# Kernel tuning notes

Hardware: AMD Instinct MI355X
Metric: run time of the kernel (lower is better)

## Reference

```python
import jax, jax.numpy as jnp
import numpy as np

HEADS = 16
EMBED = 1024
D_K = EMBED // HEADS


def setup_inputs() -> dict:
    key = jax.random.key(0)
    ks = jax.random.split(key, 11)
    B, S, E = 4, 2048, EMBED
    sc = 0.02
    return {
        "query": jax.random.normal(ks[0], (B, S, E), jnp.float32),
        "key_": jax.random.normal(ks[1], (B, S, E), jnp.float32),
        "value": jax.random.normal(ks[2], (B, S, E), jnp.float32),
        "Wq": jax.random.normal(ks[3], (E, E), jnp.float32) * sc,
        "bq": jnp.zeros((E,), jnp.float32),
        "Wk": jax.random.normal(ks[4], (E, E), jnp.float32) * sc,
        "bk": jnp.zeros((E,), jnp.float32),
        "Wv": jax.random.normal(ks[5], (E, E), jnp.float32) * sc,
        "bv": jnp.zeros((E,), jnp.float32),
        "Wo": jax.random.normal(ks[6], (E, D_K), jnp.float32) * sc,  # out: Linear(heads*d_k -> d_k)
        "bo": jnp.zeros((D_K,), jnp.float32),
    }


def reference(query, key_, value, Wq, bq, Wk, bk, Wv, bv, Wo, bo):
    B, S, E = query.shape
    H, Dk = HEADS, D_K
    # QKV projections
    q = query @ Wq + bq          # (B,S,E)
    k = key_ @ Wk + bk
    v = value @ Wv + bv
    # split heads -> (B,H,S,Dk)
    q = q.reshape(B, S, H, Dk).transpose(0, 2, 1, 3)
    k = k.reshape(B, S, H, Dk).transpose(0, 2, 1, 3)
    v = v.reshape(B, S, H, Dk).transpose(0, 2, 1, 3)
    # attention: softmax(QK^T / sqrt(d_k)) V
    scores = jnp.einsum("bhqd,bhkd->bhqk", q, k) / jnp.sqrt(jnp.asarray(Dk, q.dtype))
    attn = jax.nn.softmax(scores, axis=-1)
    ctx = jnp.einsum("bhqk,bhkd->bhqd", attn, v)
    ctx = ctx.transpose(0, 2, 1, 3).reshape(B, S, E)
    # output projection (E -> d_k, as in source)
    return ctx @ Wo + bo
```

## Files before the change

kernel.cpp:

```cpp
#include <hip/hip_runtime.h>
#include <hip/hip_bf16.h>
#include <cstdint>
#include <cstddef>

#define DEVI static __device__ __forceinline__

typedef unsigned short u16;
typedef unsigned int u32;
typedef __bf16 bf16_t;
typedef __bf16 bf16x8 __attribute__((ext_vector_type(8)));
typedef float f32x4 __attribute__((ext_vector_type(4)));
typedef float f32x16 __attribute__((ext_vector_type(16)));

union U16x8 { uint4 u; bf16x8 v; };
union PU { u32 w[4]; bf16x8 v; };

#define QSCALE 0.1803368801111204f

DEVI void gload_lds16(const void* g, void* l) {
  __builtin_amdgcn_global_load_lds((const __attribute__((address_space(1))) void*)g,
                                   (__attribute__((address_space(3))) void*)l, 16, 0, 0);
}
DEVI void wait_vmcnt0() { asm volatile("s_waitcnt vmcnt(0)" ::: "memory"); }

DEVI u32 cvt_pk_bf16(float lo, float hi) {
  u32 r;
  asm("v_cvt_pk_bf16_f32 %0, %1, %2" : "=v"(r) : "v"(lo), "v"(hi));
  return r;
}

DEVI void permswap(u32& a, u32& b) {
  asm("v_permlane32_swap_b32 %0, %1" : "+v"(a), "+v"(b));
}

DEVI f32x16 mfma32(bf16x8 a, bf16x8 b, f32x16 c) {
  return __builtin_amdgcn_mfma_f32_32x32x16_bf16(a, b, c, 0, 0, 0);
}

DEVI bf16x8 lds_frag(const char* base, int row, int koff, int swz) {
  U16x8 u;
  u.u = *(const uint4*)(base + row * 128 + (koff ^ swz));
  return u.v;
}

DEVI void transpose_body(const float* __restrict__ src, bf16_t* __restrict__ dst,
                         int R, int C, float scale, int tile, int t,
                         u16 (*tileb)[65]) {
  int tiles_c = C >> 6;
  int tc = tile % tiles_c;
  int tr = tile / tiles_c;
  int r0 = tr << 6, c0 = tc << 6;
  #pragma unroll
  for (int p = 0; p < 4; ++p) {
    int idx = t + p * 256;
    int i = idx >> 4, j4 = (idx & 15) * 4;
    float4 f = *(const float4*)(src + (size_t)(r0 + i) * C + c0 + j4);
    tileb[i][j4 + 0] = __builtin_bit_cast(u16, (bf16_t)(f.x * scale));
    tileb[i][j4 + 1] = __builtin_bit_cast(u16, (bf16_t)(f.y * scale));
    tileb[i][j4 + 2] = __builtin_bit_cast(u16, (bf16_t)(f.z * scale));
    tileb[i][j4 + 3] = __builtin_bit_cast(u16, (bf16_t)(f.w * scale));
  }
  __syncthreads();
  #pragma unroll
  for (int p = 0; p < 2; ++p) {
    int idx = t + p * 256;
    int j = idx >> 3, i0 = (idx & 7) * 8;
    u16 us[8];
    #pragma unroll
    for (int e = 0; e < 8; ++e) us[e] = tileb[i0 + e][j];
    uint4 o;
    o.x = (u32)us[0] | ((u32)us[1] << 16);
    o.y = (u32)us[2] | ((u32)us[3] << 16);
    o.z = (u32)us[4] | ((u32)us[5] << 16);
    o.w = (u32)us[6] | ((u32)us[7] << 16);
    *(uint4*)((u16*)dst + (size_t)(c0 + j) * R + r0 + i0) = o;
  }
}

__global__ __launch_bounds__(256) void k_prep(
    const float* __restrict__ qa, const float* __restrict__ ka, const float* __restrict__ va,
    const float* __restrict__ Wq, const float* __restrict__ Wk,
    const float* __restrict__ Wv, const float* __restrict__ Wo,
    bf16_t* __restrict__ Abf,
    bf16_t* __restrict__ WqT, bf16_t* __restrict__ WkT,
    bf16_t* __restrict__ WvT, bf16_t* __restrict__ WoT) {
  __shared__ u16 tileb[64][65];
  const int bid = blockIdx.x;
  const int t = threadIdx.x;
  if (bid < 3072) {
    int which = bid >> 10;
    int bb = bid & 1023;
    const float* s = which == 0 ? qa : which == 1 ? ka : va;
    u16* d = (u16*)Abf + (size_t)which * 8192 * 1024;
    size_t base = ((size_t)bb * 256 + t) * 8;
    #pragma unroll
    for (int p = 0; p < 4; ++p) {
      size_t i = base + (size_t)p * 2097152;
      float4 f0 = *(const float4*)(s + i);
      float4 f1 = *(const float4*)(s + i + 4);
      uint4 o;
      o.x = cvt_pk_bf16(f0.x, f0.y); o.y = cvt_pk_bf16(f0.z, f0.w);
      o.z = cvt_pk_bf16(f1.x, f1.y); o.w = cvt_pk_bf16(f1.z, f1.w);
      *(uint4*)(d + i) = o;
    }
  } else {
    int r = bid - 3072;
    if (r < 256)      transpose_body(Wq, WqT, 1024, 1024, QSCALE, r,       t, tileb);
    else if (r < 512) transpose_body(Wk, WkT, 1024, 1024, 1.0f,   r - 256, t, tileb);
    else if (r < 768) transpose_body(Wv, WvT, 1024, 1024, 1.0f,   r - 512, t, tileb);
    else              transpose_body(Wo, WoT, 1024, 64,   1.0f,   r - 768, t, tileb);
  }
}

template<bool PRE>
__global__ __launch_bounds__(256) void k_proj_gemm(
    const float* __restrict__ Aq, const float* __restrict__ Ak, const float* __restrict__ Av,
    const bf16_t* __restrict__ Abf,
    const bf16_t* __restrict__ WqT, const bf16_t* __restrict__ WkT, const bf16_t* __restrict__ WvT,
    const float* __restrict__ bq, const float* __restrict__ bk, const float* __restrict__ bv,
    bf16_t* __restrict__ qh, bf16_t* __restrict__ kh, bf16_t* __restrict__ vh) {
  int bx = blockIdx.x;
  int which = bx >> 9;
  int tt = bx & 511;
  int tile_m = tt & 63;
  int tile_n = tt >> 6;
  const float* A    = which == 0 ? Aq : which == 1 ? Ak : Av;
  const bf16_t* Ab  = Abf + (size_t)which * 8192 * 1024;
  const bf16_t* WT  = which == 0 ? WqT : which == 1 ? WkT : WvT;
  const float* bias = which == 0 ? bq : which == 1 ? bk : bv;
  const float bscale = which == 0 ? QSCALE : 1.0f;
  bf16_t* dst       = which == 0 ? qh : which == 1 ? kh : vh;

  const int t = threadIdx.x;
  const int l = t & 63;
  const int w = t >> 6;
  const int wm = w >> 1, wn = w & 1;
  const int c = l & 15, g = l >> 4;
  const int row0 = tile_m << 7;
  const int n0 = tile_n << 7;

  __shared__ __align__(16) char As[128 * 64 * 2];
  __shared__ __align__(16) char Bs[128 * 64 * 2];

  f32x4 acc[4][4];
  #pragma unroll
  for (int i = 0; i < 4; ++i)
    #pragma unroll
    for (int j = 0; j < 4; ++j) acc[i][j] = (f32x4){0.f, 0.f, 0.f, 0.f};

  const int arow_b = t >> 4, ac4 = t & 15;
  const float* agbase = A + (size_t)(row0 + arow_b) * 1024 + ac4 * 4;
  char* aldst = As + arow_b * 128 + (((ac4 >> 1) ^ (arow_b & 7)) << 4) + (ac4 & 1) * 8;

  for (int kt = 0; kt < 16; ++kt) {
    __syncthreads();
    if constexpr (PRE) {
      #pragma unroll
      for (int cc = 0; cc < 4; ++cc) {
        int slot = w * 256 + cc * 64 + l;
        int row = slot >> 3, chs = slot & 7;
        const bf16_t* src = Ab + (size_t)(row0 + row) * 1024 + kt * 64 + ((chs ^ (row & 7)) << 3);
        gload_lds16(src, As + (w * 256 + cc * 64) * 16);
      }
    } else {
      const float* ap = agbase + kt * 64;
      #pragma unroll
      for (int p = 0; p < 8; ++p) {
        float4 f = *(const float4*)(ap + (size_t)p * 16384);
        uint2 o;
        o.x = cvt_pk_bf16(f.x, f.y);
        o.y = cvt_pk_bf16(f.z, f.w);
        *(uint2*)(aldst + p * 2048) = o;
      }
    }
    #pragma unroll
    for (int cc = 0; cc < 4; ++cc) {
      int slot = w * 256 + cc * 64 + l;
      int row = slot >> 3, chs = slot & 7;
      const bf16_t* src = WT + (size_t)(n0 + row) * 1024 + kt * 64 + ((chs ^ (row & 7)) << 3);
      gload_lds16(src, Bs + (w * 256 + cc * 64) * 16);
    }
    wait_vmcnt0();
    __syncthreads();
    #pragma unroll
    for (int kk = 0; kk < 2; ++kk) {
      bf16x8 af[4], bfr[4];
      #pragma unroll
      for (int mi = 0; mi < 4; ++mi) {
        int row = wm * 64 + mi * 16 + c;
        U16x8 u; u.u = *(const uint4*)(As + row * 128 + ((kk * 64 + g * 16) ^ ((c & 7) << 4)));
        af[mi] = u.v;
      }
      #pragma unroll
      for (int ni = 0; ni < 4; ++ni) {
        int row = wn * 64 + ni * 16 + c;
        U16x8 u; u.u = *(const uint4*)(Bs + row * 128 + ((kk * 64 + g * 16) ^ ((c & 7) << 4)));
        bfr[ni] = u.v;
      }
      #pragma unroll
      for (int mi = 0; mi < 4; ++mi)
        #pragma unroll
        for (int ni = 0; ni < 4; ++ni)
          acc[mi][ni] = __builtin_amdgcn_mfma_f32_16x16x32_bf16(af[mi], bfr[ni], acc[mi][ni], 0, 0, 0);
    }
  }
  u16* dd = (u16*)dst;
  #pragma unroll
  for (int ni = 0; ni < 4; ++ni) {
    int col = n0 + wn * 64 + ni * 16 + c;
    float bb = bias[col] * bscale;
    int h = col >> 6, d = col & 63;
    #pragma unroll
    for (int mi = 0; mi < 4; ++mi) {
      #pragma unroll
      for (int r = 0; r < 4; ++r) {
        int rowg = row0 + wm * 64 + mi * 16 + g * 4 + r;
        int b = rowg >> 11, s = rowg & 2047;
        float vv = acc[mi][ni][r] + bb;
        size_t idx = (((size_t)b * 16 + h) * 2048 + s) * 64 + d;
        dd[idx] = __builtin_bit_cast(u16, (bf16_t)vv);
      }
    }
  }
}

__global__ __launch_bounds__(256) void k_transpose_v(
    const bf16_t* __restrict__ vh, bf16_t* __restrict__ vT) {
  int bh = blockIdx.x >> 5, st = blockIdx.x & 31;
  int s0 = st << 6;
  __shared__ __align__(16) u16 tile[64][72];
  int t = threadIdx.x;
  const u16* src = (const u16*)vh + ((size_t)bh * 2048 + s0) * 64;
  #pragma unroll
  for (int p = 0; p < 2; ++p) {
    int idx = t + p * 256;
    int s = idx >> 3, d0 = (idx & 7) * 8;
    uint4 v = *(const uint4*)(src + s * 64 + d0);
    *(uint4*)(&tile[s][d0]) = v;
  }
  __syncthreads();
  u16* dst = (u16*)vT + (size_t)bh * 64 * 2048 + s0;
  #pragma unroll
  for (int p = 0; p < 2; ++p) {
    int idx = t + p * 256;
    int d = idx >> 3, s1 = (idx & 7) * 8;
    u16 us[8];
    #pragma unroll
    for (int e = 0; e < 8; ++e) us[e] = tile[s1 + e][d];
    uint4 o;
    o.x = (u32)us[0] | ((u32)us[1] << 16);
    o.y = (u32)us[2] | ((u32)us[3] << 16);
    o.z = (u32)us[4] | ((u32)us[5] << 16);
    o.w = (u32)us[6] | ((u32)us[7] << 16);
    *(uint4*)(dst + (size_t)d * 2048 + s1) = o;
  }
}

__global__ __launch_bounds__(256, 4) void k_attn(
    const bf16_t* __restrict__ qh, const bf16_t* __restrict__ kh,
    const bf16_t* __restrict__ vT, bf16_t* __restrict__ ctx) {
  const int bid = blockIdx.x;
  const int bx = ((bid & 7) << 7) | (bid >> 3);
  const int bh = bx >> 4;
  const int qt = bx & 15;
  const int q0 = qt << 7;
  const int t = threadIdx.x, l = t & 63, w = t >> 6;
  const int q = l & 31;
  const int hi = l >> 5;
  const int swz = (q & 7) << 4;

  __shared__ __align__(16) char Ks[2][64 * 128];
  __shared__ __align__(16) char Vs[2][64 * 128];

  const u16* qrow = (const u16*)qh + ((size_t)bh * 2048 + q0 + w * 32 + q) * 64;
  bf16x8 qf0, qf1, qf2, qf3;
  {
    U16x8 u;
    u.u = *(const uint4*)(qrow + 0 * 16 + hi * 8); qf0 = u.v;
    u.u = *(const uint4*)(qrow + 1 * 16 + hi * 8); qf1 = u.v;
    u.u = *(const uint4*)(qrow + 2 * 16 + hi * 8); qf2 = u.v;
    u.u = *(const uint4*)(qrow + 3 * 16 + hi * 8); qf3 = u.v;
  }

  bf16x8 ones;
  {
    U16x8 u;
    u.u = (uint4){0x3F803F80u, 0x3F803F80u, 0x3F803F80u, 0x3F803F80u};
    ones = u.v;
  }

  const f32x16 z16 = {0.f,0.f,0.f,0.f, 0.f,0.f,0.f,0.f, 0.f,0.f,0.f,0.f, 0.f,0.f,0.f,0.f};
  f32x16 oc0 = z16, oc1 = z16, psum = z16;

  const u16* kbh = (const u16*)kh + (size_t)bh * 2048 * 64;
  const u16* vbh = (const u16*)vT + (size_t)bh * 64 * 2048;

  auto stage = [&](int kvi, int buf) {
    int kbase = kvi << 6;
    #pragma unroll
    for (int cc = 0; cc < 2; ++cc) {
      int slot = w * 128 + cc * 64 + l;
      int row = slot >> 3, chs = slot & 7;
      gload_lds16(kbh + (size_t)(kbase + row) * 64 + ((chs ^ (row & 7)) << 3),
                  Ks[buf] + (w * 128 + cc * 64) * 16);
      gload_lds16(vbh + (size_t)row * 2048 + kbase + ((chs ^ (row & 7)) << 3),
                  Vs[buf] + (w * 128 + cc * 64) * 16);
    }
  };

  stage(0, 0);
  wait_vmcnt0();
  __syncthreads();

  for (int kv = 0; kv < 32; ++kv) {
    const int cur = kv & 1;
    if (kv < 31) stage(kv + 1, cur ^ 1);
    const char* Kc = Ks[cur];
    const char* Vc = Vs[cur];

    #pragma unroll
    for (int tt = 0; tt < 2; ++tt) {
      const int arow = tt * 32 + q;
      f32x16 st = z16;
      __builtin_amdgcn_s_setprio(1);
      st = mfma32(lds_frag(Kc, arow, 0 * 32 + hi * 16, swz), qf0, st);
      st = mfma32(lds_frag(Kc, arow, 1 * 32 + hi * 16, swz), qf1, st);
      st = mfma32(lds_frag(Kc, arow, 2 * 32 + hi * 16, swz), qf2, st);
      st = mfma32(lds_frag(Kc, arow, 3 * 32 + hi * 16, swz), qf3, st);
      __builtin_amdgcn_s_setprio(0);

      float e[16];
      #pragma unroll
      for (int i = 0; i < 16; ++i) e[i] = __builtin_amdgcn_exp2f(st[i]);

      #pragma unroll
      for (int cc = 0; cc < 2; ++cc) {
        u32 a  = cvt_pk_bf16(e[8 * cc + 0], e[8 * cc + 1]);
        u32 b  = cvt_pk_bf16(e[8 * cc + 4], e[8 * cc + 5]);
        u32 c2 = cvt_pk_bf16(e[8 * cc + 2], e[8 * cc + 3]);
        u32 d  = cvt_pk_bf16(e[8 * cc + 6], e[8 * cc + 7]);
        permswap(a, b);
        permswap(c2, d);
        PU pu;
        pu.w[0] = a; pu.w[1] = c2; pu.w[2] = b; pu.w[3] = d;
        const int ks = tt * 2 + cc;
        __builtin_amdgcn_s_setprio(1);
        oc0 = mfma32(pu.v, lds_frag(Vc, q,      ks * 32 + hi * 16, swz), oc0);
        oc1 = mfma32(pu.v, lds_frag(Vc, 32 + q, ks * 32 + hi * 16, swz), oc1);
        psum = mfma32(pu.v, ones, psum);
        __builtin_amdgcn_s_setprio(0);
      }
    }
    wait_vmcnt0();
    __syncthreads();
  }

  const int b = bh >> 4, hh = bh & 15;
  u16* cb = (u16*)ctx;
  #pragma unroll
  for (int qd = 0; qd < 4; ++qd) {
    #pragma unroll
    for (int r = 0; r < 4; ++r) {
      float inv = 1.f / psum[qd * 4 + r];
      int qrow_g = q0 + w * 32 + qd * 8 + hi * 4 + r;
      size_t base = ((size_t)b * 2048 + qrow_g) * 1024 + hh * 64;
      float v0 = oc0[qd * 4 + r] * inv;
      float v1 = oc1[qd * 4 + r] * inv;
      cb[base + q]      = __builtin_bit_cast(u16, (bf16_t)v0);
      cb[base + 32 + q] = __builtin_bit_cast(u16, (bf16_t)v1);
    }
  }
}

__global__ __launch_bounds__(256) void k_out_gemm(
    const bf16_t* __restrict__ ctx, const bf16_t* __restrict__ WoT,
    const float* __restrict__ bo, float* __restrict__ out) {
  int tile_m = blockIdx.x;
  const int t = threadIdx.x, l = t & 63, w = t >> 6;
  const int wm = w >> 1, wn = w & 1;
  const int c = l & 15, g = l >> 4;
  const int row0 = tile_m << 7;

  __shared__ __align__(16) char As[128 * 64 * 2];
  __shared__ __align__(16) char Bs[64 * 64 * 2];

  f32x4 acc[4][2];
  #pragma unroll
  for (int i = 0; i < 4; ++i)
    #pragma unroll
    for (int j = 0; j < 2; ++j) acc[i][j] = (f32x4){0.f, 0.f, 0.f, 0.f};

  for (int kt = 0; kt < 16; ++kt) {
    __syncthreads();
    #pragma unroll
    for (int cc = 0; cc < 4; ++cc) {
      int slot = w * 256 + cc * 64 + l;
      int row = slot >> 3, chs = slot & 7;
      const bf16_t* src = ctx + (size_t)(row0 + row) * 1024 + kt * 64 + ((chs ^ (row & 7)) << 3);
      gload_lds16(src, As + (w * 256 + cc * 64) * 16);
    }
    #pragma unroll
    for (int cc = 0; cc < 2; ++cc) {
      int slot = w * 128 + cc * 64 + l;
      int row = slot >> 3, chs = slot & 7;
      const bf16_t* src = WoT + (size_t)row * 1024 + kt * 64 + ((chs ^ (row & 7)) << 3);
      gload_lds16(src, Bs + (w * 128 + cc * 64) * 16);
    }
    wait_vmcnt0();
    __syncthreads();
    #pragma unroll
    for (int kk = 0; kk < 2; ++kk) {
      bf16x8 af[4], bfr[2];
      #pragma unroll
      for (int mi = 0; mi < 4; ++mi) {
        int row = wm * 64 + mi * 16 + c;
        U16x8 u; u.u = *(const uint4*)(As + row * 128 + ((kk * 64 + g * 16) ^ ((c & 7) << 4)));
        af[mi] = u.v;
      }
      #pragma unroll
      for (int ni = 0; ni < 2; ++ni) {
        int row = wn * 32 + ni * 16 + c;
        U16x8 u; u.u = *(const uint4*)(Bs + row * 128 + ((kk * 64 + g * 16) ^ ((c & 7) << 4)));
        bfr[ni] = u.v;
      }
      #pragma unroll
      for (int mi = 0; mi < 4; ++mi)
        #pragma unroll
        for (int ni = 0; ni < 2; ++ni)
          acc[mi][ni] = __builtin_amdgcn_mfma_f32_16x16x32_bf16(af[mi], bfr[ni], acc[mi][ni], 0, 0, 0);
    }
  }
  #pragma unroll
  for (int ni = 0; ni < 2; ++ni) {
    int col = wn * 32 + ni * 16 + c;
    float bb = bo[col];
    #pragma unroll
    for (int mi = 0; mi < 4; ++mi) {
      #pragma unroll
      for (int r = 0; r < 4; ++r) {
        int rowg = row0 + wm * 64 + mi * 16 + g * 4 + r;
        out[(size_t)rowg * 64 + col] = acc[mi][ni][r] + bb;
      }
    }
  }
}

extern "C" void kernel_launch(void* const* d_in, const int* in_sizes, int n_in,
                              void* d_out, int out_size, void* d_ws, size_t ws_size,
                              hipStream_t stream) {
  (void)in_sizes; (void)n_in; (void)out_size;
  const float* query = (const float*)d_in[0];
  const float* key_  = (const float*)d_in[1];
  const float* value = (const float*)d_in[2];
  const float* Wq = (const float*)d_in[3];
  const float* bq = (const float*)d_in[4];
  const float* Wk = (const float*)d_in[5];
  const float* bk = (const float*)d_in[6];
  const float* Wv = (const float*)d_in[7];
  const float* bv = (const float*)d_in[8];
  const float* Wo = (const float*)d_in[9];
  const float* bo = (const float*)d_in[10];
  float* out = (float*)d_out;

  char* ws = (char*)d_ws;
  bf16_t* WqT = (bf16_t*)(ws + (size_t)0);
  bf16_t* WkT = (bf16_t*)(ws + ((size_t)2 << 20));
  bf16_t* WvT = (bf16_t*)(ws + ((size_t)4 << 20));
  bf16_t* WoT = (bf16_t*)(ws + ((size_t)6 << 20));
  bf16_t* qhd = (bf16_t*)(ws + ((size_t)8 << 20));
  bf16_t* khd = (bf16_t*)(ws + ((size_t)24 << 20));
  bf16_t* vhd = (bf16_t*)(ws + ((size_t)40 << 20));
  bf16_t* vT  = (bf16_t*)(ws + ((size_t)56 << 20));
  bf16_t* ctx = (bf16_t*)(ws + ((size_t)72 << 20));
  bf16_t* Abf = (bf16_t*)(ws + ((size_t)88 << 20));

  const bool pre = ws_size >= ((size_t)137 << 20);

  if (pre) {
    k_prep<<<3856, 256, 0, stream>>>(query, key_, value, Wq, Wk, Wv, Wo,
                                     Abf, WqT, WkT, WvT, WoT);
    k_proj_gemm<true><<<1536, 256, 0, stream>>>(query, key_, value, Abf, WqT, WkT, WvT,
                                                bq, bk, bv, qhd, khd, vhd);
  } else {
    k_prep<<<3856, 256, 0, stream>>>(query, key_, value, Wq, Wk, Wv, Wo,
                                     Abf, WqT, WkT, WvT, WoT);
    k_proj_gemm<false><<<1536, 256, 0, stream>>>(query, key_, value, Abf, WqT, WkT, WvT,
                                                 bq, bk, bv, qhd, khd, vhd);
  }
  k_transpose_v<<<2048, 256, 0, stream>>>(vhd, vT);
  k_attn<<<1024, 256, 0, stream>>>(qhd, khd, vT, ctx);
  k_out_gemm<<<64, 256, 0, stream>>>(ctx, WoT, bo, out);
}
```

Baseline: 194.7 us.

## Fuse V transpose into projection epilogue and shrink output GEMM tiles

The QKV projection epilogue now writes V directly in the transposed (d-major) layout with packed 4-element stores, which removes the separate V transpose kernel and its extra global round trip. The output GEMM uses 32-row tiles instead of 128, launching 256 blocks rather than 64 to fill more compute units. The trade-off is less operand reuse per wave in the output GEMM, plus strided stores in the V epilogue.

Measured after the change: 186.4 us. 4.3% less time.

```diff
diff --git a/kernel.cpp b/kernel.cpp
--- a/kernel.cpp
+++ b/kernel.cpp
@@ -118,7 +118,7 @@
     const bf16_t* __restrict__ Abf,
     const bf16_t* __restrict__ WqT, const bf16_t* __restrict__ WkT, const bf16_t* __restrict__ WvT,
     const float* __restrict__ bq, const float* __restrict__ bk, const float* __restrict__ bv,
-    bf16_t* __restrict__ qh, bf16_t* __restrict__ kh, bf16_t* __restrict__ vh) {
+    bf16_t* __restrict__ qh, bf16_t* __restrict__ kh, bf16_t* __restrict__ vT) {
   int bx = blockIdx.x;
   int which = bx >> 9;
   int tt = bx & 511;
@@ -129,7 +129,6 @@
   const bf16_t* WT  = which == 0 ? WqT : which == 1 ? WkT : WvT;
   const float* bias = which == 0 ? bq : which == 1 ? bk : bv;
   const float bscale = which == 0 ? QSCALE : 1.0f;
-  bf16_t* dst       = which == 0 ? qh : which == 1 ? kh : vh;
 
   const int t = threadIdx.x;
   const int l = t & 63;
@@ -204,55 +203,45 @@
           acc[mi][ni] = __builtin_amdgcn_mfma_f32_16x16x32_bf16(af[mi], bfr[ni], acc[mi][ni], 0, 0, 0);
     }
   }
-  u16* dd = (u16*)dst;
-  #pragma unroll
-  for (int ni = 0; ni < 4; ++ni) {
-    int col = n0 + wn * 64 + ni * 16 + c;
-    float bb = bias[col] * bscale;
-    int h = col >> 6, d = col & 63;
-    #pragma unroll
-    for (int mi = 0; mi < 4; ++mi) {
-      #pragma unroll
-      for (int r = 0; r < 4; ++r) {
-        int rowg = row0 + wm * 64 + mi * 16 + g * 4 + r;
-        int b = rowg >> 11, s = rowg & 2047;
-        float vv = acc[mi][ni][r] + bb;
-        size_t idx = (((size_t)b * 16 + h) * 2048 + s) * 64 + d;
-        dd[idx] = __builtin_bit_cast(u16, (bf16_t)vv);
-      }
-    }
-  }
-}
-
-__global__ __launch_bounds__(256) void k_transpose_v(
-    const bf16_t* __restrict__ vh, bf16_t* __restrict__ vT) {
-  int bh = blockIdx.x >> 5, st = blockIdx.x & 31;
-  int s0 = st << 6;
-  __shared__ __align__(16) u16 tile[64][72];
-  int t = threadIdx.x;
-  const u16* src = (const u16*)vh + ((size_t)bh * 2048 + s0) * 64;
-  #pragma unroll
-  for (int p = 0; p < 2; ++p) {
-    int idx = t + p * 256;
-    int s = idx >> 3, d0 = (idx & 7) * 8;
-    uint4 v = *(const uint4*)(src + s * 64 + d0);
-    *(uint4*)(&tile[s][d0]) = v;
-  }
-  __syncthreads();
-  u16* dst = (u16*)vT + (size_t)bh * 64 * 2048 + s0;
-  #pragma unroll
-  for (int p = 0; p < 2; ++p) {
-    int idx = t + p * 256;
-    int d = idx >> 3, s1 = (idx & 7) * 8;
-    u16 us[8];
-    #pragma unroll
-    for (int e = 0; e < 8; ++e) us[e] = tile[s1 + e][d];
-    uint4 o;
-    o.x = (u32)us[0] | ((u32)us[1] << 16);
-    o.y = (u32)us[2] | ((u32)us[3] << 16);
-    o.z = (u32)us[4] | ((u32)us[5] << 16);
-    o.w = (u32)us[6] | ((u32)us[7] << 16);
-    *(uint4*)(dst + (size_t)d * 2048 + s1) = o;
+
+  const int b = row0 >> 11;
+  const int sl0 = row0 & 2047;
+  if (which == 2) {
+    u16* vbase = (u16*)vT;
+    #pragma unroll
+    for (int ni = 0; ni < 4; ++ni) {
+      int col = n0 + wn * 64 + ni * 16 + c;
+      float bb = bias[col];
+      int h = col >> 6, d = col & 63;
+      u16* rowp = vbase + (((size_t)(b * 16 + h) * 64 + d) * 2048);
+      #pragma unroll
+      for (int mi = 0; mi < 4; ++mi) {
+        int s = sl0 + wm * 64 + mi * 16 + g * 4;
+        uint2 pv;
+        pv.x = cvt_pk_bf16(acc[mi][ni][0] + bb, acc[mi][ni][1] + bb);
+        pv.y = cvt_pk_bf16(acc[mi][ni][2] + bb, acc[mi][ni][3] + bb);
+        *(uint2*)(rowp + s) = pv;
+      }
+    }
+  } else {
+    bf16_t* dst = which == 0 ? qh : kh;
+    u16* dd = (u16*)dst;
+    #pragma unroll
+    for (int ni = 0; ni < 4; ++ni) {
+      int col = n0 + wn * 64 + ni * 16 + c;
+      float bb = bias[col] * bscale;
+      int h = col >> 6, d = col & 63;
+      #pragma unroll
+      for (int mi = 0; mi < 4; ++mi) {
+        #pragma unroll
+        for (int r = 0; r < 4; ++r) {
+          int s = sl0 + wm * 64 + mi * 16 + g * 4 + r;
+          float vv = acc[mi][ni][r] + bb;
+          size_t idx = (((size_t)b * 16 + h) * 2048 + s) * 64 + d;
+          dd[idx] = __builtin_bit_cast(u16, (bf16_t)vv);
+        }
+      }
+    }
   }
 }
 
@@ -379,25 +368,21 @@
   const int t = threadIdx.x, l = t & 63, w = t >> 6;
   const int wm = w >> 1, wn = w & 1;
   const int c = l & 15, g = l >> 4;
-  const int row0 = tile_m << 7;
-
-  __shared__ __align__(16) char As[128 * 64 * 2];
+  const int row0 = tile_m << 5;
+
+  __shared__ __align__(16) char As[32 * 64 * 2];
   __shared__ __align__(16) char Bs[64 * 64 * 2];
 
-  f32x4 acc[4][2];
-  #pragma unroll
-  for (int i = 0; i < 4; ++i)
-    #pragma unroll
-    for (int j = 0; j < 2; ++j) acc[i][j] = (f32x4){0.f, 0.f, 0.f, 0.f};
+  f32x4 acc[2];
+  acc[0] = (f32x4){0.f, 0.f, 0.f, 0.f};
+  acc[1] = (f32x4){0.f, 0.f, 0.f, 0.f};
 
   for (int kt = 0; kt < 16; ++kt) {
     __syncthreads();
-    #pragma unroll
-    for (int cc = 0; cc < 4; ++cc) {
-      int slot = w * 256 + cc * 64 + l;
-      int row = slot >> 3, chs = slot & 7;
+    {
+      int row = t >> 3, chs = t & 7;
       const bf16_t* src = ctx + (size_t)(row0 + row) * 1024 + kt * 64 + ((chs ^ (row & 7)) << 3);
-      gload_lds16(src, As + (w * 256 + cc * 64) * 16);
+      gload_lds16(src, As + t * 16);
     }
     #pragma unroll
     for (int cc = 0; cc < 2; ++cc) {
@@ -410,24 +395,18 @@
     __syncthreads();
     #pragma unroll
     for (int kk = 0; kk < 2; ++kk) {
-      bf16x8 af[4], bfr[2];
-      #pragma unroll
-      for (int mi = 0; mi < 4; ++mi) {
-        int row = wm * 64 + mi * 16 + c;
+      bf16x8 af;
+      {
+        int row = wm * 16 + c;
         U16x8 u; u.u = *(const uint4*)(As + row * 128 + ((kk * 64 + g * 16) ^ ((c & 7) << 4)));
-        af[mi] = u.v;
+        af = u.v;
       }
       #pragma unroll
       for (int ni = 0; ni < 2; ++ni) {
         int row = wn * 32 + ni * 16 + c;
         U16x8 u; u.u = *(const uint4*)(Bs + row * 128 + ((kk * 64 + g * 16) ^ ((c & 7) << 4)));
-        bfr[ni] = u.v;
-      }
-      #pragma unroll
-      for (int mi = 0; mi < 4; ++mi)
-        #pragma unroll
-        for (int ni = 0; ni < 2; ++ni)
-          acc[mi][ni] = __builtin_amdgcn_mfma_f32_16x16x32_bf16(af[mi], bfr[ni], acc[mi][ni], 0, 0, 0);
+        acc[ni] = __builtin_amdgcn_mfma_f32_16x16x32_bf16(af, u.v, acc[ni], 0, 0, 0);
+      }
     }
   }
   #pragma unroll
@@ -435,12 +414,9 @@
     int col = wn * 32 + ni * 16 + c;
     float bb = bo[col];
     #pragma unroll
-    for (int mi = 0; mi < 4; ++mi) {
-      #pragma unroll
-      for (int r = 0; r < 4; ++r) {
-        int rowg = row0 + wm * 64 + mi * 16 + g * 4 + r;
-        out[(size_t)rowg * 64 + col] = acc[mi][ni][r] + bb;
-      }
+    for (int r = 0; r < 4; ++r) {
+      int rowg = row0 + wm * 16 + g * 4 + r;
+      out[(size_t)rowg * 64 + col] = acc[ni][r] + bb;
     }
   }
 }
@@ -469,25 +445,21 @@
   bf16_t* WoT = (bf16_t*)(ws + ((size_t)6 << 20));
   bf16_t* qhd = (bf16_t*)(ws + ((size_t)8 << 20));
   bf16_t* khd = (bf16_t*)(ws + ((size_t)24 << 20));
-  bf16_t* vhd = (bf16_t*)(ws + ((size_t)40 << 20));
   bf16_t* vT  = (bf16_t*)(ws + ((size_t)56 << 20));
   bf16_t* ctx = (bf16_t*)(ws + ((size_t)72 << 20));
   bf16_t* Abf = (bf16_t*)(ws + ((size_t)88 << 20));
 
   const bool pre = ws_size >= ((size_t)137 << 20);
 
+  k_prep<<<3856, 256, 0, stream>>>(query, key_, value, Wq, Wk, Wv, Wo,
+                                   Abf, WqT, WkT, WvT, WoT);
   if (pre) {
-    k_prep<<<3856, 256, 0, stream>>>(query, key_, value, Wq, Wk, Wv, Wo,
-                                     Abf, WqT, WkT, WvT, WoT);
     k_proj_gemm<true><<<1536, 256, 0, stream>>>(query, key_, value, Abf, WqT, WkT, WvT,
-                                                bq, bk, bv, qhd, khd, vhd);
+                                                bq, bk, bv, qhd, khd, vT);
   } else {
-    k_prep<<<3856, 256, 0, stream>>>(query, key_, value, Wq, Wk, Wv, Wo,
-                                     Abf, WqT, WkT, WvT, WoT);
     k_proj_gemm<false><<<1536, 256, 0, stream>>>(query, key_, value, Abf, WqT, WkT, WvT,
-                                                 bq, bk, bv, qhd, khd, vhd);
-  }
-  k_transpose_v<<<2048, 256, 0, stream>>>(vhd, vT);
+                                                 bq, bk, bv, qhd, khd, vT);
+  }
   k_attn<<<1024, 256, 0, stream>>>(qhd, khd, vT, ctx);
-  k_out_gemm<<<64, 256, 0, stream>>>(ctx, WoT, bo, out);
-}
+  k_out_gemm<<<256, 256, 0, stream>>>(ctx, WoT, bo, out);
+}
```
